# Performance work log

Measured on AMD Instinct MI355X. Metric: run time of the kernel, lower is better.

Reference implementation:

```python
import jax, jax.numpy as jnp
import numpy as np
from jax import lax

B, NPG, IN, OUT, ETYPES, STEPS, E = 16, 1024, 128, 256, 2, 6, 262144
N = B * NPG
CONCAT = IN + OUT
EPS = 1e-5


def setup_inputs() -> dict:
    key = jax.random.key(0)
    ks = jax.random.split(key, 24)
    s = 0.05
    return {
        "features": jax.random.normal(ks[0], (N, IN), jnp.float32),
        "src": jax.random.randint(ks[1], (E,), 0, N, jnp.int32),
        "dst": jax.random.randint(ks[2], (E,), 0, N, jnp.int32),
        "etype": jax.random.randint(ks[3], (E,), 0, ETYPES, jnp.int32),
        # GGNN per-etype linears (weight, bias) and GRUCell params
        "W_lin": jax.random.normal(ks[4], (ETYPES, OUT, OUT), jnp.float32) * s,
        "b_lin": jnp.zeros((ETYPES, OUT), jnp.float32),
        "W_ih": jax.random.normal(ks[5], (3 * OUT, OUT), jnp.float32) * s,
        "W_hh": jax.random.normal(ks[6], (3 * OUT, OUT), jnp.float32) * s,
        "b_ih": jnp.zeros((3 * OUT,), jnp.float32),
        "b_hh": jnp.zeros((3 * OUT,), jnp.float32),
        # conv branch on h_i (OUT channels)
        "conv1_w": jax.random.normal(ks[7], (OUT, OUT, 3), jnp.float32) * s,
        "conv1_b": jnp.zeros((OUT,), jnp.float32),
        "conv2_w": jax.random.normal(ks[8], (OUT, OUT, 1), jnp.float32) * s,
        "conv2_b": jnp.zeros((OUT,), jnp.float32),
        # conv branch on c_i (CONCAT channels)
        "convc1_w": jax.random.normal(ks[9], (CONCAT, CONCAT, 3), jnp.float32) * s,
        "convc1_b": jnp.zeros((CONCAT,), jnp.float32),
        "convc2_w": jax.random.normal(ks[10], (CONCAT, CONCAT, 1), jnp.float32) * s,
        "convc2_b": jnp.zeros((CONCAT,), jnp.float32),
        # shared batchnorms (training-mode batch stats, affine params)
        "bn_g": jnp.ones((OUT,), jnp.float32),
        "bn_b": jnp.zeros((OUT,), jnp.float32),
        "bnc_g": jnp.ones((CONCAT,), jnp.float32),
        "bnc_b": jnp.zeros((CONCAT,), jnp.float32),
        # gating MLPs
        "mlpy_w": jax.random.normal(ks[11], (2, OUT), jnp.float32) * s,
        "mlpy_b": jnp.zeros((2,), jnp.float32),
        "mlpz_w": jax.random.normal(ks[12], (2, CONCAT), jnp.float32) * s,
        "mlpz_b": jnp.zeros((2,), jnp.float32),
    }


def _bn_relu(x, g, b):  # x: [B, C, L], training-mode BN (biased var)
    mean = x.mean(axis=(0, 2), keepdims=True)
    var = ((x - mean) ** 2).mean(axis=(0, 2), keepdims=True)
    xn = (x - mean) * lax.rsqrt(var + EPS)
    return jax.nn.relu(xn * g[None, :, None] + b[None, :, None])


def _conv1d(x, w, b):  # x: [B, C, L], w: [O, I, K]
    y = lax.conv_general_dilated(x, w, (1,), 'VALID',
                                 dimension_numbers=('NCH', 'OIH', 'NCH'))
    return y + b[None, :, None]


def _maxpool(x, k, s):
    return lax.reduce_window(x, -jnp.inf, lax.max, (1, 1, k), (1, 1, s), 'VALID')


def _forward(features, src, dst, etype, W_lin, b_lin, W_ih, W_hh, b_ih, b_hh,
             conv1_w, conv1_b, conv2_w, conv2_b, convc1_w, convc1_b,
             convc2_w, convc2_b, bn_g, bn_b, bnc_g, bnc_b,
             mlpy_w, mlpy_b, mlpz_w, mlpz_b):
    # --- GatedGraphConv (DGL semantics): pad, n_steps of msg-pass + GRUCell ---
    h = jnp.pad(features, ((0, 0), (0, OUT - IN)))  # [N, OUT]
    for _ in range(STEPS):
        # per-etype linear applied to all nodes: [ETYPES, N, OUT]
        Wh = jnp.einsum('nd,ekd->enk', h, W_lin) + b_lin[:, None, :]
        msg = Wh[etype, src]                              # [E, OUT] gather
        agg = jax.ops.segment_sum(msg, dst, num_segments=N)  # scatter-add
        gi = agg @ W_ih.T + b_ih
        gh = h @ W_hh.T + b_hh
        ir, iz, ig = jnp.split(gi, 3, axis=-1)
        hr, hz, hg = jnp.split(gh, 3, axis=-1)
        r = jax.nn.sigmoid(ir + hr)
        z = jax.nn.sigmoid(iz + hz)
        n = jnp.tanh(ig + r * hg)
        h = (1.0 - z) * n + z * h

    h_i = h.reshape(B, NPG, OUT)
    x_i = features.reshape(B, NPG, IN)
    c_i = jnp.concatenate([h_i, x_i], axis=-1)  # [B, NPG, CONCAT]

    hT = jnp.swapaxes(h_i, 1, 2)  # [B, OUT, NPG]
    Y1 = _maxpool(_bn_relu(_conv1d(hT, conv1_w, conv1_b), bn_g, bn_b), 3, 2)
    Y2 = jnp.swapaxes(_maxpool(_bn_relu(_conv1d(Y1, conv2_w, conv2_b), bn_g, bn_b), 2, 2), 1, 2)

    cT = jnp.swapaxes(c_i, 1, 2)  # [B, CONCAT, NPG]
    Z1 = _maxpool(_bn_relu(_conv1d(cT, convc1_w, convc1_b), bnc_g, bnc_b), 3, 2)
    Z2 = jnp.swapaxes(_maxpool(_bn_relu(_conv1d(Z1, convc2_w, convc2_b), bnc_g, bnc_b), 2, 2), 1, 2)

    before_avg = (Y2 @ mlpy_w.T + mlpy_b) * (Z2 @ mlpz_w.T + mlpz_b)  # [B, L, 2]
    return jax.nn.sigmoid(before_avg.mean(axis=1))  # [B, 2]


def reference(features, src, dst, etype, W_lin, b_lin, W_ih, W_hh, b_ih, b_hh,
              conv1_w, conv1_b, conv2_w, conv2_b, convc1_w, convc1_b,
              convc2_w, convc2_b, bn_g, bn_b, bnc_g, bnc_b,
              mlpy_w, mlpy_b, mlpz_w, mlpz_b):
    return _forward(features, src, dst, etype, W_lin, b_lin, W_ih, W_hh, b_ih, b_hh,
                    conv1_w, conv1_b, conv2_w, conv2_b, convc1_w, convc1_b,
                    convc2_w, convc2_b, bn_g, bn_b, bnc_g, bnc_b,
                    mlpy_w, mlpy_b, mlpz_w, mlpz_b)
```

## Files before the change

kernel.cpp:

```cpp
#include <hip/hip_runtime.h>
#include <math.h>

constexpr int Bn     = 16;
constexpr int NPG    = 1024;
constexpr int Nn     = Bn * NPG;
constexpr int FIN    = 128;
constexpr int FOUT   = 256;
constexpr int CCAT   = 384;
constexpr int STEPS  = 6;
constexpr int NE     = 262144;

using short8 = __attribute__((ext_vector_type(8))) short;
using f32x4  = __attribute__((ext_vector_type(4))) float;

static __device__ __forceinline__ unsigned short f2bf(float x) {
    union { float f; unsigned u; } v; v.f = x;
    unsigned r = (v.u + 0x7FFFu + ((v.u >> 16) & 1u)) >> 16;
    return (unsigned short)r;
}
static __device__ __forceinline__ float bf2f(unsigned short b) {
    union { unsigned u; float f; } v; v.u = ((unsigned)b) << 16;
    return v.f;
}
static __device__ __forceinline__ float sigm(float x) { return 1.f / (1.f + expf(-x)); }

static __device__ __forceinline__ void gload16(const void* g, void* l) {
    __builtin_amdgcn_global_load_lds(
        (const __attribute__((address_space(1))) void*)g,
        (__attribute__((address_space(3))) void*)l, 16, 0, 0);
}


__global__ void cvt_bf(const float* __restrict__ s, unsigned short* __restrict__ d, int n) {
    int i = blockIdx.x * 256 + threadIdx.x;
    if (i < n) d[i] = f2bf(s[i]);
}

__global__ void cvt_wcat(const float* __restrict__ Wih, const float* __restrict__ Whh,
                         unsigned short* __restrict__ Wcat) {
    int o = blockIdx.x * 256 + threadIdx.x;
    int k = o >> 9, j = o & 511;
    float v = (j < 256) ? Whh[(size_t)k * 256 + j] : Wih[(size_t)k * 256 + (j - 256)];
    Wcat[o] = f2bf(v);
}

__global__ void add_bias(const float* __restrict__ a, const float* __restrict__ b,
                         float* __restrict__ o, int n) {
    int i = blockIdx.x * 256 + threadIdx.x;
    if (i < n) o[i] = a[i] + b[i];
}

__global__ void cvt_wconv(const float* __restrict__ W, unsigned short* __restrict__ Wt,
                          int C, int KW, int n) {
    int o = blockIdx.x * 256 + threadIdx.x;
    if (o >= n) return;
    int c = o / (KW * C), rem = o % (KW * C);
    int kb = rem / C, i = rem % C;
    Wt[o] = f2bf(W[(size_t)(c * C + i) * KW + kb]);
}

__global__ void pad_h(const float* __restrict__ f, float* __restrict__ h,
                      unsigned short* __restrict__ Acat) {
    int i = blockIdx.x * 256 + threadIdx.x;
    int k = i & 255, n = i >> 8;
    float v = (k < FIN) ? f[(size_t)n * FIN + k] : 0.f;
    h[i] = v; Acat[(size_t)n * 512 + k] = f2bf(v);
}

__global__ void build_cb(const unsigned short* __restrict__ Acat, const float* __restrict__ f,
                         unsigned short* __restrict__ cb) {
    int idx = blockIdx.x * 256 + threadIdx.x;
    int c = idx % CCAT, n = idx / CCAT;
    cb[idx] = (c < FOUT) ? Acat[(size_t)n * 512 + c] : f2bf(f[(size_t)n * FIN + (c - FOUT)]);
}


__global__ void edge_count(const int* __restrict__ dst, int* __restrict__ deg) {
    int e = blockIdx.x * 256 + threadIdx.x;
    atomicAdd(&deg[dst[e]], 1);
}

__global__ __launch_bounds__(1024) void scan_deg(const int* __restrict__ deg,
                                                 int* __restrict__ rowptr,
                                                 int* __restrict__ cursor) {
    __shared__ int ps[1024];
    const int t = threadIdx.x;
    int loc[16]; int s = 0;
    const int base = t * 16;
#pragma unroll
    for (int i = 0; i < 16; ++i) { loc[i] = deg[base + i]; s += loc[i]; }
    ps[t] = s;
    __syncthreads();
    for (int off = 1; off < 1024; off <<= 1) {
        int add = (t >= off) ? ps[t - off] : 0;
        __syncthreads();
        ps[t] += add;
        __syncthreads();
    }
    int run = ps[t] - s;
#pragma unroll
    for (int i = 0; i < 16; ++i) { rowptr[base + i] = run; cursor[base + i] = run; run += loc[i]; }
    if (t == 1023) rowptr[16384] = run;
}

__global__ void edge_fill(const int* __restrict__ src, const int* __restrict__ dst,
                          const int* __restrict__ et, int* __restrict__ cursor,
                          int* __restrict__ widx) {
    int e = blockIdx.x * 256 + threadIdx.x;
    int slot = atomicAdd(&cursor[dst[e]], 1);
    widx[slot] = src[e] * 2 + et[e];
}

static __device__ __forceinline__ void gemm128_body(
    const unsigned short* __restrict__ Ab, const unsigned short* __restrict__ W,
    const float* __restrict__ bias, float* __restrict__ Cf,
    unsigned short* __restrict__ Cb, int Ctap, int lda, int L, int Lv, int N, int K,
    int outBf, int l0, int col0, unsigned short* As, unsigned short* Bs) {
    const int t = threadIdx.x;
    const int w = t >> 6, l = t & 63;
    const int lr = l & 15, lhi = l >> 4;
    const int wr = w >> 1, wc = w & 1;
    const int srow8 = l >> 3;
    const int scole = ((l & 7) ^ srow8) * 8;
    const int lx7 = l & 7;

    f32x4 acc[4][4] = {};

    for (int k0 = 0; k0 < K; k0 += 64) {
        const int kb = k0 / Ctap;
        const int i0 = k0 - kb * Ctap;
        __syncthreads();
#pragma unroll
        for (int p = 0; p < 4; ++p) {
            const int r = w * 32 + p * 8;
            int srow = l0 + r + srow8 + kb;
            srow = srow < L ? srow : L - 1;
            gload16(Ab + (size_t)srow * lda + i0 + scole, &As[r * 64]);
            gload16(W + (size_t)(col0 + r + srow8) * K + k0 + scole, &Bs[r * 64]);
        }
        __syncthreads();
        const int abase = (wr * 64 + lr) * 64;
        const int bbase = (wc * 64 + lr) * 64;
#pragma unroll
        for (int kk = 0; kk < 2; ++kk) {
            const int soff = ((kk * 4 + lhi) ^ lx7) * 8;
            short8 af[4], bw[4];
#pragma unroll
            for (int fi = 0; fi < 4; ++fi)
                af[fi] = *(const short8*)&As[abase + fi * 1024 + soff];
#pragma unroll
            for (int fj = 0; fj < 4; ++fj)
                bw[fj] = *(const short8*)&Bs[bbase + fj * 1024 + soff];
#pragma unroll
            for (int fi = 0; fi < 4; ++fi)
#pragma unroll
                for (int fj = 0; fj < 4; ++fj)
                    acc[fi][fj] = __builtin_amdgcn_mfma_f32_16x16x32_bf16(
                        af[fi], bw[fj], acc[fi][fj], 0, 0, 0);
        }
    }
    const int rb = lhi * 4;
#pragma unroll
    for (int fi = 0; fi < 4; ++fi)
#pragma unroll
        for (int fj = 0; fj < 4; ++fj) {
            const int gcol = col0 + wc * 64 + fj * 16 + lr;
            const float bv = bias[gcol];
#pragma unroll
            for (int rr = 0; rr < 4; ++rr) {
                const int grow = l0 + wr * 64 + fi * 16 + rb + rr;
                if (grow < Lv) {
                    float v = acc[fi][fj][rr] + bv;
                    const size_t o = (size_t)grow * N + gcol;
                    if (outBf) Cb[o] = f2bf(v);
                    else       Cf[o] = v;
                }
            }
        }
}

__global__ __launch_bounds__(256) void gemm128_swz(
    const unsigned short* __restrict__ A, const unsigned short* __restrict__ W,
    const float* __restrict__ bias, unsigned short* __restrict__ Cb,
    int lda, int N, int K) {
    __shared__ unsigned short As[128 * 64];
    __shared__ unsigned short Bs[128 * 64];
    const int gX = gridDim.x;
    const int hId = blockIdx.x + gX * blockIdx.y;
    const int xcd = hId & 7, tt = hId >> 3;
    const int bx = tt % gX, by = xcd + 8 * (tt / gX);
    gemm128_body(A, W, bias, nullptr, Cb, lda, lda, Nn, Nn, N, K, 1,
                 by * 128, bx * 128, As, Bs);
}

__global__ __launch_bounds__(256) void gemm128_pair2(
    const unsigned short* __restrict__ A1, const unsigned short* __restrict__ W1,
    const float* __restrict__ b1, unsigned short* __restrict__ C1,
    int Ctap1, int lda1, int L1, int Lv1, int N1, int K1, int nx1, int ny1,
    const unsigned short* __restrict__ A2, const unsigned short* __restrict__ W2,
    const float* __restrict__ b2, unsigned short* __restrict__ C2,
    int Ctap2, int lda2, int L2, int Lv2, int N2, int K2, int nx2, int ny2) {
    __shared__ unsigned short As[128 * 64];
    __shared__ unsigned short Bs[128 * 64];
    const int G = gridDim.x;
    int id = (blockIdx.x & 7) * (G >> 3) + (blockIdx.x >> 3);
    const int n1 = nx1 * ny1 * Bn;
    if (id < n1) {
        int x = id % nx1, y = (id / nx1) % ny1, z = id / (nx1 * ny1);
        gemm128_body(A1 + (size_t)z * L1 * lda1, W1, b1, nullptr,
                     C1 + (size_t)z * Lv1 * N1,
                     Ctap1, lda1, L1, Lv1, N1, K1, 1, y * 128, x * 128, As, Bs);
    } else {
        id -= n1;
        int x = id % nx2, y = (id / nx2) % ny2, z = id / (nx2 * ny2);
        gemm128_body(A2 + (size_t)z * L2 * lda2, W2, b2, nullptr,
                     C2 + (size_t)z * Lv2 * N2,
                     Ctap2, lda2, L2, Lv2, N2, K2, 1, y * 128, x * 128, As, Bs);
    }
}

__global__ __launch_bounds__(256) void gemm_gru(
    const unsigned short* __restrict__ Acat, const unsigned short* __restrict__ Wcat,
    const unsigned short* __restrict__ Whg, const float* __restrict__ bias_s,
    const float* __restrict__ bias_g, float* __restrict__ h,
    unsigned short* __restrict__ Anext) {
    __shared__ unsigned short As[64 * 64];
    __shared__ unsigned short Bs[256 * 64];
    const int hId = blockIdx.x + 4 * blockIdx.y;
    const int xcd = hId & 7, tt = hId >> 3;
    const int bx = tt & 3, by = xcd + 8 * (tt >> 2);
    const int l0 = by * 64, c0 = bx * 64;

    const int t = threadIdx.x;
    const int w = t >> 6, l = t & 63;
    const int lr = l & 15, lhi = l >> 4;
    const int srow8 = l >> 3;
    const int scole = ((l & 7) ^ srow8) * 8;
    const int lx7 = l & 7;

    f32x4 acc[16] = {};

#pragma unroll
    for (int k0 = 0; k0 < 512; k0 += 64) {
        __syncthreads();
#pragma unroll
        for (int p = 0; p < 2; ++p) {
            const int r = w * 16 + p * 8;
            gload16(Acat + (size_t)(l0 + r + srow8) * 512 + k0 + scole, &As[r * 64]);
        }
#pragma unroll
        for (int p = 0; p < 8; ++p) {
            const int r = w * 64 + p * 8;
            if (r < 192) {
                const int g = r >> 6;
                const int cr = (r & 63) + srow8;
                gload16(Wcat + (size_t)(g * 256 + c0 + cr) * 512 + k0 + scole, &Bs[r * 64]);
            } else if (k0 < 256) {
                const int cr = (r - 192) + srow8;
                gload16(Whg + (size_t)(c0 + cr) * 256 + k0 + scole, &Bs[r * 64]);
            }
        }
        __syncthreads();
        const int abase = (w * 16 + lr) * 64;
#pragma unroll
        for (int kk = 0; kk < 2; ++kk) {
            const int soff = ((kk * 4 + lhi) ^ lx7) * 8;
            short8 a0 = *(const short8*)&As[abase + soff];
#pragma unroll
            for (int g = 0; g < 4; ++g) {
                if (!(g == 3 && k0 >= 256)) {
#pragma unroll
                    for (int fj = 0; fj < 4; ++fj) {
                        short8 bb = *(const short8*)&Bs[(g * 64 + fj * 16 + lr) * 64 + soff];
                        acc[g * 4 + fj] = __builtin_amdgcn_mfma_f32_16x16x32_bf16(
                            a0, bb, acc[g * 4 + fj], 0, 0, 0);
                    }
                }
            }
        }
    }
    const int rb = lhi * 4;
#pragma unroll
    for (int fj = 0; fj < 4; ++fj) {
        const int c = c0 + fj * 16 + lr;
        const float br = bias_s[c];
        const float bz = bias_s[256 + c];
        const float bg = bias_s[512 + c];
        const float bh = bias_g[c];
#pragma unroll
        for (int rr = 0; rr < 4; ++rr) {
            const int grow = l0 + w * 16 + rb + rr;
            float sr = acc[0 * 4 + fj][rr] + br;
            float sz = acc[1 * 4 + fj][rr] + bz;
            float sg = acc[2 * 4 + fj][rr] + bg;
            float hg = acc[3 * 4 + fj][rr] + bh;
            float r = sigm(sr), z = sigm(sz);
            float nn = tanhf(sg - (1.f - r) * hg);
            const size_t ho = (size_t)grow * 256 + c;
            float hv = (1.f - z) * nn + z * h[ho];
            h[ho] = hv;
            Anext[(size_t)grow * 512 + c] = f2bf(hv);
        }
    }
}

__global__ __launch_bounds__(256) void gather_agg(
    const unsigned short* __restrict__ Whb, const int* __restrict__ rowptr,
    const int* __restrict__ widx, unsigned short* __restrict__ Acat) {
    const int n = blockIdx.x * 4 + (threadIdx.x >> 6);
    const int t = threadIdx.x & 63;
    const int s0 = rowptr[n], s1 = rowptr[n + 1];
    float p0[4] = {}, p1[4] = {}, p2[4] = {}, p3[4] = {};
    int s = s0;
    for (; s + 4 <= s1; s += 4) {
        const int w0 = widx[s], w1 = widx[s + 1], w2 = widx[s + 2], w3 = widx[s + 3];
        const ushort4 v0 = *(const ushort4*)(Whb + (size_t)w0 * 256 + t * 4);
        const ushort4 v1 = *(const ushort4*)(Whb + (size_t)w1 * 256 + t * 4);
        const ushort4 v2 = *(const ushort4*)(Whb + (size_t)w2 * 256 + t * 4);
        const ushort4 v3 = *(const ushort4*)(Whb + (size_t)w3 * 256 + t * 4);
        p0[0] += bf2f(v0.x); p0[1] += bf2f(v0.y); p0[2] += bf2f(v0.z); p0[3] += bf2f(v0.w);
        p1[0] += bf2f(v1.x); p1[1] += bf2f(v1.y); p1[2] += bf2f(v1.z); p1[3] += bf2f(v1.w);
        p2[0] += bf2f(v2.x); p2[1] += bf2f(v2.y); p2[2] += bf2f(v2.z); p2[3] += bf2f(v2.w);
        p3[0] += bf2f(v3.x); p3[1] += bf2f(v3.y); p3[2] += bf2f(v3.z); p3[3] += bf2f(v3.w);
    }
    for (; s < s1; ++s) {
        const int wi = widx[s];
        const ushort4 v = *(const ushort4*)(Whb + (size_t)wi * 256 + t * 4);
        p0[0] += bf2f(v.x); p0[1] += bf2f(v.y); p0[2] += bf2f(v.z); p0[3] += bf2f(v.w);
    }
    ushort4 o;
    o.x = f2bf(p0[0] + p1[0] + p2[0] + p3[0]);
    o.y = f2bf(p0[1] + p1[1] + p2[1] + p3[1]);
    o.z = f2bf(p0[2] + p1[2] + p2[2] + p3[2]);
    o.w = f2bf(p0[3] + p1[3] + p2[3] + p3[3]);
    *(ushort4*)(Acat + (size_t)n * 512 + 256 + t * 4) = o;
}

constexpr int NCHUNK = 128;

static __device__ __forceinline__ void bn_part_body(
    const unsigned short* __restrict__ X, float* __restrict__ pS, float* __restrict__ pQ,
    int C, int totalRows, int rowsPerChunk, int bx, int by) {
    const int t  = threadIdx.x;
    const int cq = t & 31, rl = t >> 5;
    const int c0 = bx * 128 + cq * 4;
    const int r0 = by * rowsPerChunk;
    const int r1 = min(r0 + rowsPerChunk, totalRows);
    float s0 = 0, s1 = 0, s2 = 0, s3 = 0, q0 = 0, q1 = 0, q2 = 0, q3 = 0;
    for (int r = r0 + rl; r < r1; r += 8) {
        ushort4 u = *(const ushort4*)(X + (size_t)r * C + c0);
        float v0 = bf2f(u.x), v1 = bf2f(u.y), v2 = bf2f(u.z), v3 = bf2f(u.w);
        s0 += v0; s1 += v1; s2 += v2; s3 += v3;
        q0 += v0 * v0; q1 += v1 * v1; q2 += v2 * v2; q3 += v3 * v3;
    }
    __shared__ float ls[8][128], lq[8][128];
    ls[rl][cq * 4 + 0] = s0; ls[rl][cq * 4 + 1] = s1;
    ls[rl][cq * 4 + 2] = s2; ls[rl][cq * 4 + 3] = s3;
    lq[rl][cq * 4 + 0] = q0; lq[rl][cq * 4 + 1] = q1;
    lq[rl][cq * 4 + 2] = q2; lq[rl][cq * 4 + 3] = q3;
    __syncthreads();
    if (rl == 0) {
#pragma unroll
        for (int i = 0; i < 4; ++i) {
            const int c = cq * 4 + i;
            float ss = 0, qq = 0;
#pragma unroll
            for (int j = 0; j < 8; ++j) { ss += ls[j][c]; qq += lq[j][c]; }
            pS[(size_t)by * C + c0 + i] = ss;
            pQ[(size_t)by * C + c0 + i] = qq;
        }
    }
}

__global__ __launch_bounds__(256) void bn_part_pair(
    const unsigned short* __restrict__ X1, float* __restrict__ pS1, float* __restrict__ pQ1, int C1,
    const unsigned short* __restrict__ X2, float* __restrict__ pS2, float* __restrict__ pQ2, int C2,
    int totalRows, int rowsPerChunk) {
    int id = blockIdx.x;
    const int n1 = (C1 / 128) * NCHUNK;
    if (id < n1)
        bn_part_body(X1, pS1, pQ1, C1, totalRows, rowsPerChunk, id % (C1 / 128), id / (C1 / 128));
    else {
        id -= n1;
        bn_part_body(X2, pS2, pQ2, C2, totalRows, rowsPerChunk, id % (C2 / 128), id / (C2 / 128));
    }
}

__global__ __launch_bounds__(128) void bn_reduce_pair(
    const float* __restrict__ pS1, const float* __restrict__ pQ1,
    float* __restrict__ mean1, float* __restrict__ var1, int C1,
    const float* __restrict__ pS2, const float* __restrict__ pQ2,
    float* __restrict__ mean2, float* __restrict__ var2, int C2, int totalRows) {
    int c = blockIdx.x;
    const float* pS; const float* pQ; float* mean; float* var; int C;
    if (c < C1) { pS = pS1; pQ = pQ1; mean = mean1; var = var1; C = C1; }
    else { c -= C1; pS = pS2; pQ = pQ2; mean = mean2; var = var2; C = C2; }
    const int t = threadIdx.x;
    __shared__ float rs[128], rq[128];
    rs[t] = pS[(size_t)t * C + c];
    rq[t] = pQ[(size_t)t * C + c];
    __syncthreads();
    for (int st = 64; st; st >>= 1) {
        if (t < st) { rs[t] += rs[t + st]; rq[t] += rq[t + st]; }
        __syncthreads();
    }
    if (t == 0) {
        float m = rs[0] / totalRows;
        mean[c] = m;
        var[c]  = rq[0] / totalRows - m * m;
    }
}

static __device__ __forceinline__ void bnp_body(
    const unsigned short* __restrict__ X, const float* __restrict__ mean,
    const float* __restrict__ var, const float* __restrict__ g,
    const float* __restrict__ bta, float* __restrict__ Of,
    unsigned short* __restrict__ Ob, int C, int Lin, int Lout, int Kp, int outBf, int idx) {
    if (idx >= Bn * Lout * C) return;
    int c = idx % C, j = (idx / C) % Lout, b = idx / (C * Lout);
    float sc = g[c] * rsqrtf(var[c] + 1e-5f);
    float sh = bta[c] - mean[c] * sc;
    const unsigned short* xb = X + ((size_t)b * Lin + j * 2) * C + c;
    float m = 0.f;
    for (int k = 0; k < Kp; ++k) m = fmaxf(m, bf2f(xb[(size_t)k * C]) * sc + sh);
    if (outBf) Ob[idx] = f2bf(m);
    else       Of[idx] = m;
}

__global__ void bnp_pair(
    const unsigned short* __restrict__ X1, const float* __restrict__ mean1,
    const float* __restrict__ var1, const float* __restrict__ g1,
    const float* __restrict__ b1, float* __restrict__ Of1,
    unsigned short* __restrict__ Ob1, int C1,
    const unsigned short* __restrict__ X2, const float* __restrict__ mean2,
    const float* __restrict__ var2, const float* __restrict__ g2,
    const float* __restrict__ b2, float* __restrict__ Of2,
    unsigned short* __restrict__ Ob2, int C2,
    int Lin, int Lout, int Kp, int outBf) {
    int id = blockIdx.x;
    const int nb1 = (Bn * Lout * C1 + 255) / 256;
    if (id < nb1)
        bnp_body(X1, mean1, var1, g1, b1, Of1, Ob1, C1, Lin, Lout, Kp, outBf,
                 id * 256 + threadIdx.x);
    else
        bnp_body(X2, mean2, var2, g2, b2, Of2, Ob2, C2, Lin, Lout, Kp, outBf,
                 (id - nb1) * 256 + threadIdx.x);
}

__global__ void final_dot(const float* __restrict__ Y2, const float* __restrict__ Z2,
                          const float* __restrict__ wy, const float* __restrict__ by,
                          const float* __restrict__ wz, const float* __restrict__ bz,
                          float* __restrict__ prod) {
    const int b = blockIdx.y, j = blockIdx.x, t = threadIdx.x;
    float p0 = 0, p1 = 0, q0 = 0, q1 = 0;
    const float* yrow = Y2 + (size_t)(b * 255 + j) * FOUT;
    const float* zrow = Z2 + (size_t)(b * 255 + j) * CCAT;
    for (int c = t; c < FOUT; c += 128) {
        float v = yrow[c];
        p0 += v * wy[c]; p1 += v * wy[FOUT + c];
    }
    for (int c = t; c < CCAT; c += 128) {
        float v = zrow[c];
        q0 += v * wz[c]; q1 += v * wz[CCAT + c];
    }
    __shared__ float r0[128], r1[128], r2[128], r3[128];
    r0[t] = p0; r1[t] = p1; r2[t] = q0; r3[t] = q1;
    __syncthreads();
    for (int s = 64; s; s >>= 1) {
        if (t < s) { r0[t] += r0[t + s]; r1[t] += r1[t + s]; r2[t] += r2[t + s]; r3[t] += r3[t + s]; }
        __syncthreads();
    }
    if (t == 0) {
        float y0 = r0[0] + by[0], y1 = r1[0] + by[1];
        float z0 = r2[0] + bz[0], z1 = r3[0] + bz[1];
        prod[((size_t)b * 255 + j) * 2 + 0] = y0 * z0;
        prod[((size_t)b * 255 + j) * 2 + 1] = y1 * z1;
    }
}

__global__ void final_out(const float* __restrict__ prod, float* __restrict__ out) {
    const int b = blockIdx.x, t = threadIdx.x;
    const int w = t >> 6, lane = t & 63;
    float s = 0.f;
    for (int j = lane; j < 255; j += 64) s += prod[((size_t)b * 255 + j) * 2 + w];
#pragma unroll
    for (int off = 32; off; off >>= 1) s += __shfl_down(s, off);
    if (lane == 0) out[b * 2 + w] = 1.f / (1.f + expf(-s / 255.f));
}

extern "C" void kernel_launch(void* const* d_in, const int* in_sizes, int n_in,
                              void* d_out, int out_size, void* d_ws, size_t ws_size,
                              hipStream_t stream) {
    (void)in_sizes; (void)n_in; (void)out_size; (void)ws_size;
    const float* features = (const float*)d_in[0];
    const int*   src      = (const int*)d_in[1];
    const int*   dst      = (const int*)d_in[2];
    const int*   etype    = (const int*)d_in[3];
    const float* W_lin    = (const float*)d_in[4];
    const float* b_lin    = (const float*)d_in[5];
    const float* W_ih     = (const float*)d_in[6];
    const float* W_hh     = (const float*)d_in[7];
    const float* b_ih     = (const float*)d_in[8];
    const float* b_hh     = (const float*)d_in[9];
    const float* conv1_w  = (const float*)d_in[10];
    const float* conv1_b  = (const float*)d_in[11];
    const float* conv2_w  = (const float*)d_in[12];
    const float* conv2_b  = (const float*)d_in[13];
    const float* convc1_w = (const float*)d_in[14];
    const float* convc1_b = (const float*)d_in[15];
    const float* convc2_w = (const float*)d_in[16];
    const float* convc2_b = (const float*)d_in[17];
    const float* bn_g     = (const float*)d_in[18];
    const float* bn_b     = (const float*)d_in[19];
    const float* bnc_g    = (const float*)d_in[20];
    const float* bnc_b    = (const float*)d_in[21];
    const float* mlpy_w   = (const float*)d_in[22];
    const float* mlpy_b   = (const float*)d_in[23];
    const float* mlpz_w   = (const float*)d_in[24];
    const float* mlpz_b   = (const float*)d_in[25];

    float* ws = (float*)d_ws;
    float*          h      = ws;
    unsigned short* Acat0  = (unsigned short*)(ws + 4194304);
    float*          bufA   = ws + 8388608;
    float*          bufB   = ws + 20971520;
    unsigned short* Wlin_b = (unsigned short*)(ws + 33554432);
    unsigned short* Whh_b  = (unsigned short*)(ws + 33554432) + 131072;
    unsigned short* Wcat_b = (unsigned short*)(ws + 33554432) + 327680;
    float*          bias_s = ws + 33950000;
    int*            ib     = (int*)(ws + 34000000);
    int* deg    = ib;
    int* cursor = ib + 16384;
    int* rowptr = ib + 32768;
    int* widx   = ib + 49160;
    float* sreg = ws + 34500000;
    float* meanY = sreg;
    float* varY  = sreg + 256;
    float* meanZ = sreg + 512;
    float* varZ  = sreg + 896;
    float* pSy   = sreg + 1280;
    float* pQy   = sreg + 34048;
    float* pSz   = sreg + 66816;
    float* pQz   = sreg + 115968;
    float* prod  = sreg + 165120;

    unsigned short* Whb   = (unsigned short*)bufA;
    unsigned short* Acat1 = (unsigned short*)(bufA + 4194304);
    const unsigned short* Whg = Whh_b + 512 * 256;

    cvt_bf<<<512,  256, 0, stream>>>(W_lin, Wlin_b, 131072);
    cvt_bf<<<768,  256, 0, stream>>>(W_hh,  Whh_b,  196608);
    cvt_wcat<<<1536, 256, 0, stream>>>(W_ih, W_hh, Wcat_b);
    add_bias<<<3, 256, 0, stream>>>(b_ih, b_hh, bias_s, 768);
    pad_h<<<Nn * FOUT / 256, 256, 0, stream>>>(features, h, Acat0);

    hipMemsetAsync(deg, 0, 16384 * sizeof(int), stream);
    edge_count<<<NE / 256, 256, 0, stream>>>(dst, deg);
    scan_deg<<<1, 1024, 0, stream>>>(deg, rowptr, cursor);
    edge_fill<<<NE / 256, 256, 0, stream>>>(src, dst, etype, cursor, widx);

    unsigned short* Acur = Acat0;
    unsigned short* Anxt = Acat1;
    for (int s6 = 0; s6 < STEPS; ++s6) {
        gemm128_swz<<<dim3(4, 128), 256, 0, stream>>>(
            Acur, Wlin_b, b_lin, Whb, 512, 512, 256);
        gather_agg<<<Nn / 4, 256, 0, stream>>>(Whb, rowptr, widx, Acur);
        gemm_gru<<<dim3(4, 256), 256, 0, stream>>>(
            Acur, Wcat_b, Whg, bias_s, b_hh + 512, h, Anxt);
        unsigned short* tmp = Acur; Acur = Anxt; Anxt = tmp;
    }

    unsigned short* cb    = (unsigned short*)ws;
    unsigned short* Yc1   = (unsigned short*)bufA;
    unsigned short* P1y   = (unsigned short*)(bufA + 4186112);
    unsigned short* Yc2   = (unsigned short*)(bufA + 5230592);
    float*          Y2    = bufA + 7319552;
    float*          Z2    = bufA + 8364032;
    unsigned short* Zc1   = (unsigned short*)bufB;
    unsigned short* P1z   = (unsigned short*)(bufB + 6279168);
    unsigned short* Zc2   = (unsigned short*)(bufB + 7845888);
    unsigned short* Wcv   = (unsigned short*)(bufB + 11000000);
    unsigned short* c1b   = Wcv;
    unsigned short* c2b   = Wcv + 196608;
    unsigned short* cc1b  = Wcv + 262144;
    unsigned short* cc2b  = Wcv + 704512;

    cvt_wconv<<<768,  256, 0, stream>>>(conv1_w,  c1b,  FOUT, 3, FOUT * FOUT * 3);
    cvt_wconv<<<256,  256, 0, stream>>>(conv2_w,  c2b,  FOUT, 1, FOUT * FOUT);
    cvt_wconv<<<1728, 256, 0, stream>>>(convc1_w, cc1b, CCAT, 3, CCAT * CCAT * 3);
    cvt_wconv<<<576,  256, 0, stream>>>(convc2_w, cc2b, CCAT, 1, CCAT * CCAT);
    build_cb<<<Nn * CCAT / 256, 256, 0, stream>>>(Acat0, features, cb);

    const int rows1 = Bn * 1022;
    const int rows2 = Bn * 510;
    const int rpc1  = (rows1 + NCHUNK - 1) / NCHUNK;
    const int rpc2  = (rows2 + NCHUNK - 1) / NCHUNK;

    gemm128_pair2<<<2 * 8 * Bn + 3 * 8 * Bn, 256, 0, stream>>>(
        Acat0, c1b, conv1_b, Yc1, FOUT, 512, 1024, 1022, FOUT, 768, 2, 8,
        cb, cc1b, convc1_b, Zc1, CCAT, 384, 1024, 1022, CCAT, 1152, 3, 8);
    bn_part_pair<<<(2 + 3) * NCHUNK, 256, 0, stream>>>(
        Yc1, pSy, pQy, FOUT, Zc1, pSz, pQz, CCAT, rows1, rpc1);
    bn_reduce_pair<<<FOUT + CCAT, 128, 0, stream>>>(
        pSy, pQy, meanY, varY, FOUT, pSz, pQz, meanZ, varZ, CCAT, rows1);
    {
        const int nb1 = (Bn * 510 * FOUT + 255) / 256;
        const int nb2 = (Bn * 510 * CCAT + 255) / 256;
        bnp_pair<<<nb1 + nb2, 256, 0, stream>>>(
            Yc1, meanY, varY, bn_g, bn_b, nullptr, P1y, FOUT,
            Zc1, meanZ, varZ, bnc_g, bnc_b, nullptr, P1z, CCAT, 1022, 510, 3, 1);
    }

    gemm128_pair2<<<2 * 4 * Bn + 3 * 4 * Bn, 256, 0, stream>>>(
        P1y, c2b, conv2_b, Yc2, FOUT, 256, 510, 510, FOUT, 256, 2, 4,
        P1z, cc2b, convc2_b, Zc2, CCAT, 384, 510, 510, CCAT, 384, 3, 4);
    bn_part_pair<<<(2 + 3) * NCHUNK, 256, 0, stream>>>(
        Yc2, pSy, pQy, FOUT, Zc2, pSz, pQz, CCAT, rows2, rpc2);
    bn_reduce_pair<<<FOUT + CCAT, 128, 0, stream>>>(
        pSy, pQy, meanY, varY, FOUT, pSz, pQz, meanZ, varZ, CCAT, rows2);
    {
        const int nb1 = (Bn * 255 * FOUT + 255) / 256;
        const int nb2 = (Bn * 255 * CCAT + 255) / 256;
        bnp_pair<<<nb1 + nb2, 256, 0, stream>>>(
            Yc2, meanY, varY, bn_g, bn_b, Y2, nullptr, FOUT,
            Zc2, meanZ, varZ, bnc_g, bnc_b, Z2, nullptr, CCAT, 510, 255, 2, 0);
    }

    final_dot<<<dim3(255, Bn), 128, 0, stream>>>(Y2, Z2, mlpy_w, mlpy_b, mlpz_w, mlpz_b, prod);
    final_out<<<Bn, 128, 0, stream>>>(prod, (float*)d_out);
}
```

Baseline: 611.7 us.

## Double-buffer LDS tiles in GRU GEMM to overlap global loads with MFMA

Makes the shared-memory A and B tiles of the fused GRU GEMM double-buffered and prefetches the next K-slice while MFMAs run on the current one. Explicit vmcnt waits and s_barriers replace the paired __syncthreads. To keep the load count uniform, the Whg rows are always loaded, with K wrapped mod 256, even when they go unused. This doubles LDS use (about 80KB per block), which may lower occupancy, and the hand-tuned vmcnt(10) assumes an exact per-stage load count.

```diff
diff --git a/kernel.cpp b/kernel.cpp
--- a/kernel.cpp
+++ b/kernel.cpp
@@ -224,8 +224,8 @@
     const unsigned short* __restrict__ Whg, const float* __restrict__ bias_s,
     const float* __restrict__ bias_g, float* __restrict__ h,
     unsigned short* __restrict__ Anext) {
-    __shared__ unsigned short As[64 * 64];
-    __shared__ unsigned short Bs[256 * 64];
+    __shared__ unsigned short As[2][64 * 64];
+    __shared__ unsigned short Bs[2][256 * 64];
     const int hId = blockIdx.x + 4 * blockIdx.y;
     const int xcd = hId & 7, tt = hId >> 3;
     const int bx = tt & 3, by = xcd + 8 * (tt >> 2);
@@ -240,45 +240,68 @@
 
     f32x4 acc[16] = {};
 
-#pragma unroll
-    for (int k0 = 0; k0 < 512; k0 += 64) {
-        __syncthreads();
-#pragma unroll
-        for (int p = 0; p < 2; ++p) {
-            const int r = w * 16 + p * 8;
-            gload16(Acat + (size_t)(l0 + r + srow8) * 512 + k0 + scole, &As[r * 64]);
-        }
-#pragma unroll
-        for (int p = 0; p < 8; ++p) {
-            const int r = w * 64 + p * 8;
-            if (r < 192) {
-                const int g = r >> 6;
-                const int cr = (r & 63) + srow8;
-                gload16(Wcat + (size_t)(g * 256 + c0 + cr) * 512 + k0 + scole, &Bs[r * 64]);
-            } else if (k0 < 256) {
-                const int cr = (r - 192) + srow8;
-                gload16(Whg + (size_t)(c0 + cr) * 256 + k0 + scole, &Bs[r * 64]);
-            }
-        }
-        __syncthreads();
+#define STAGE_GRU(K0V, BUF)                                                          \
+    {                                                                                \
+        const int _k0 = (K0V);                                                       \
+        _Pragma("unroll")                                                            \
+        for (int p = 0; p < 2; ++p) {                                                \
+            const int r = w * 16 + p * 8;                                            \
+            gload16(Acat + (size_t)(l0 + r + srow8) * 512 + _k0 + scole,             \
+                    &As[BUF][r * 64]);                                               \
+        }                                                                            \
+        _Pragma("unroll")                                                            \
+        for (int p = 0; p < 8; ++p) {                                                \
+            const int r = w * 64 + p * 8;                          \
+            if (r < 192) {                                                           \
+                const int g = r >> 6;                                                \
+                const int cr = (r & 63) + srow8;                                     \
+                gload16(Wcat + (size_t)(g * 256 + c0 + cr) * 512 + _k0 + scole,      \
+                        &Bs[BUF][r * 64]);                                           \
+            } else {                                                                 \
+                const int cr = (r - 192) + srow8;                                    \
+                gload16(Whg + (size_t)(c0 + cr) * 256 + (_k0 & 255) + scole,         \
+                        &Bs[BUF][r * 64]);       \
+            }                                                                        \
+        }                                                                            \
+    }
+
+    STAGE_GRU(0, 0);
+    __builtin_amdgcn_sched_barrier(0);
+
+#pragma unroll
+    for (int k = 0; k < 8; ++k) {
+        const int cur = k & 1;
+        if (k < 7) { STAGE_GRU((k + 1) * 64, cur ^ 1); }
+        __builtin_amdgcn_sched_barrier(0);
+        if (k < 7) asm volatile("s_waitcnt vmcnt(10)" ::: "memory");
+        else       asm volatile("s_waitcnt vmcnt(0)" ::: "memory");
+        __builtin_amdgcn_s_barrier();
+        __builtin_amdgcn_sched_barrier(0);
+        const int k0 = k * 64;
         const int abase = (w * 16 + lr) * 64;
 #pragma unroll
         for (int kk = 0; kk < 2; ++kk) {
             const int soff = ((kk * 4 + lhi) ^ lx7) * 8;
-            short8 a0 = *(const short8*)&As[abase + soff];
+            short8 a0 = *(const short8*)&As[cur][abase + soff];
 #pragma unroll
             for (int g = 0; g < 4; ++g) {
                 if (!(g == 3 && k0 >= 256)) {
 #pragma unroll
                     for (int fj = 0; fj < 4; ++fj) {
-                        short8 bb = *(const short8*)&Bs[(g * 64 + fj * 16 + lr) * 64 + soff];
+                        short8 bb = *(const short8*)&Bs[cur][(g * 64 + fj * 16 + lr) * 64 + soff];
                         acc[g * 4 + fj] = __builtin_amdgcn_mfma_f32_16x16x32_bf16(
                             a0, bb, acc[g * 4 + fj], 0, 0, 0);
                     }
                 }
             }
         }
-    }
+        __builtin_amdgcn_sched_barrier(0);
+        asm volatile("s_waitcnt lgkmcnt(0)" ::: "memory");
+        __builtin_amdgcn_sched_barrier(0);
+        __builtin_amdgcn_s_barrier();
+    }
+#undef STAGE_GRU
+
     const int rb = lhi * 4;
 #pragma unroll
     for (int fj = 0; fj < 4; ++fj) {
```

After: 630.6 us. 3.1% more time.
